# Kernel optimization log

Hardware: AMD Instinct MI355X
Metric: run time of the kernel (lower is better)

The kernel has to match this reference:

```python
import jax, jax.numpy as jnp
import numpy as np

B, T, E = 4, 2048, 2048
H, KV = 16, 4
G = H // KV           # GQA group size
D = E // H            # head_dim = 128


def setup_inputs() -> dict:
    key = jax.random.key(0)
    kx, kq, kk, kv, ko = jax.random.split(key, 5)
    s = 1.0 / np.sqrt(E).astype(np.float32)
    x  = jax.random.normal(kx, (B, T, E), jnp.float32)
    Wq = jax.random.normal(kq, (E, H * D), jnp.float32) * s
    Wk = jax.random.normal(kk, (E, KV * D), jnp.float32) * s
    Wv = jax.random.normal(kv, (E, KV * D), jnp.float32) * s
    Wo = jax.random.normal(ko, (H * D, E), jnp.float32) * s
    return {"x": x, "Wq": Wq, "Wk": Wk, "Wv": Wv, "Wo": Wo}


def reference(x, Wq, Wk, Wv, Wo):
    # causal=True (default in the torch module)
    b, t, _ = x.shape
    scale = 1.0 / np.sqrt(D).astype(np.float32)
    # q heads ordered so that reshape (H,)->(KV,G) matches torch repeat_interleave
    q = (x @ Wq).reshape(b, t, KV, G, D)   # (B,T,KV,G,D)
    k = (x @ Wk).reshape(b, t, KV, D)      # (B,T,KV,D)
    v = (x @ Wv).reshape(b, t, KV, D)
    # scores per (kv-head h, group member g): (B,KV,G,T,T)
    scores = jnp.einsum('bqhgd,bkhd->bhgqk', q, k) * scale
    causal_mask = jnp.tril(jnp.ones((t, t), dtype=bool))  # True = keep
    scores = jnp.where(causal_mask, scores, -jnp.inf)
    w = jax.nn.softmax(scores, axis=-1)
    y = jnp.einsum('bhgqk,bkhd->bqhgd', w, v)  # (B,T,KV,G,D)
    y = y.reshape(b, t, H * D)
    return y @ Wo
```

## Files before the change

### kernel.cpp

```cpp
#include <hip/hip_runtime.h>

typedef unsigned short u16;
typedef __attribute__((ext_vector_type(8))) __bf16 bf16x8;
typedef __attribute__((ext_vector_type(4))) float f32x4;

#define BB 4
#define TT 2048
#define EE 2048
#define HH 16
#define KVH 4
#define DD 128

static __device__ __forceinline__ u16 f2bf(float f) {
  unsigned int u = __float_as_uint(f);
  u += 0x7fffu + ((u >> 16) & 1u);
  return (u16)(u >> 16);
}

static __device__ __forceinline__ void gl_lds16(const u16* g, u16* l) {
  __builtin_amdgcn_global_load_lds((__attribute__((address_space(1))) void*)g,
                                   (__attribute__((address_space(3))) void*)l,
                                   16, 0, 0);
}

__global__ __launch_bounds__(256) void cvt_f32_bf16(const float* __restrict__ in,
                                                    u16* __restrict__ out, int n4) {
  int i = blockIdx.x * 256 + threadIdx.x;
  if (i >= n4) return;
  float4 v = ((const float4*)in)[i];
  union { uint2 u2; u16 s[4]; } o;
  o.s[0] = f2bf(v.x); o.s[1] = f2bf(v.y); o.s[2] = f2bf(v.z); o.s[3] = f2bf(v.w);
  ((uint2*)out)[i] = o.u2;
}

__global__ __launch_bounds__(256) void transpose_w(const float* __restrict__ W,
                                                   u16* __restrict__ Wt, int R, int C) {
  __shared__ float tile[32][33];
  int tx = threadIdx.x & 31, ty = threadIdx.x >> 5;
  int r0 = blockIdx.y * 32, c0 = blockIdx.x * 32;
  #pragma unroll
  for (int i = ty; i < 32; i += 8)
    tile[i][tx] = W[(size_t)(r0 + i) * C + (c0 + tx)];
  __syncthreads();
  #pragma unroll
  for (int i = ty; i < 32; i += 8)
    Wt[(size_t)(c0 + i) * R + (r0 + tx)] = f2bf(tile[tx][i]);
}

__global__ __launch_bounds__(256) void transpose_v(const u16* __restrict__ KVb,
                                                   u16* __restrict__ VTg) {
  __shared__ u16 tile[32][36];
  const int tid = threadIdx.x;
  const int t0 = blockIdx.x * 32, d0 = blockIdx.y * 32;
  const int z = blockIdx.z;
  const int vb = z * 128;
  const size_t srcbase = (size_t)(z >> 2) * TT * 1024 + 512 + (z & 3) * 128;
  {
    int i = tid >> 3, c4 = (tid & 7) * 4;
    union { uint2 u; u16 s[4]; } r;
    r.u = *(const uint2*)(KVb + srcbase + (size_t)(t0 + i) * 1024 + d0 + c4);
    tile[i][c4] = r.s[0]; tile[i][c4 + 1] = r.s[1];
    tile[i][c4 + 2] = r.s[2]; tile[i][c4 + 3] = r.s[3];
  }
  __syncthreads();
  {
    int j = tid >> 3, cc = (tid & 7) * 4;
    union { uint2 u; u16 s[4]; } w;
    w.s[0] = tile[cc][j]; w.s[1] = tile[cc + 1][j];
    w.s[2] = tile[cc + 2][j]; w.s[3] = tile[cc + 3][j];
    *(uint2*)(VTg + (size_t)(vb + d0 + j) * TT + t0 + cc) = w.u;
  }
}

template <int MODE>
__global__ __launch_bounds__(512) void gemm256(const u16* __restrict__ A,
                                               const u16* __restrict__ Bt0,
                                               const u16* __restrict__ Bt1,
                                               void* __restrict__ C0,
                                               void* __restrict__ C1,
                                               int M, int N0, int N1, int K, int nbx) {
  __shared__ __align__(16) u16 sh[2][4][8192];
  const int tid = threadIdx.x;
  const int lane = tid & 63, wave = tid >> 6;
  const int quad = lane >> 4, n16 = lane & 15;
  const int mi = wave >> 2, ni = wave & 3;

  const int nwg = gridDim.x;
  int wg = blockIdx.x;
  wg = (wg & 7) * (nwg >> 3) + (wg >> 3);
  const int bx = wg % nbx, by = wg / nbx;
  const size_t rowbase = (size_t)by * 256;
  const int colbase = bx * 256;

  const u16* Bt = Bt0;
  int bcol = colbase;
  if (MODE == 1 && colbase >= N0) { Bt = Bt1; bcol = colbase - N0; }

  const int c0 = tid, c1 = tid + 512;
  const int r0s = c0 >> 3, ci0 = (c0 & 7) ^ (r0s & 7);
  const int r1s = c1 >> 3, ci1 = (c1 & 7) ^ (r1s & 7);
  const u16* Ag0 = A + (rowbase + r0s) * (size_t)K + ci0 * 8;
  const u16* Ag1 = A + (rowbase + r1s) * (size_t)K + ci1 * 8;
  const u16* Bg0 = Bt + ((size_t)bcol + r0s) * K + ci0 * 8;
  const u16* Bg1 = Bt + ((size_t)bcol + r1s) * K + ci1 * 8;
  const size_t h128K = (size_t)128 * K;

#define STAGE(ob, h, kb) do {                                              \
    if ((h) < 2) {                                                         \
      gl_lds16(Ag0 + (size_t)(h) * h128K + (kb), &sh[ob][h][c0 * 8]);      \
      gl_lds16(Ag1 + (size_t)(h) * h128K + (kb), &sh[ob][h][c1 * 8]);      \
    } else {                                                               \
      gl_lds16(Bg0 + (size_t)((h) - 2) * h128K + (kb), &sh[ob][h][c0 * 8]);\
      gl_lds16(Bg1 + (size_t)((h) - 2) * h128K + (kb), &sh[ob][h][c1 * 8]);\
    } } while (0)

#define LDA_HALF(mh) do {                                                  \
    _Pragma("unroll") for (int m = 0; m < 4; ++m)                          \
      _Pragma("unroll") for (int kk = 0; kk < 2; ++kk) {                   \
        int row_ = ((mh) * 4 + m) * 16 + n16;                              \
        int c_ = row_ * 8 + ((kk * 4 + quad) ^ (n16 & 7));                 \
        af[m][kk] = *(const bf16x8*)&sh[buf][mi][c_ * 8];                  \
      } } while (0)

#define LDB_HALF(nh, BF) do {                                              \
    _Pragma("unroll") for (int n = 0; n < 2; ++n)                          \
      _Pragma("unroll") for (int kk = 0; kk < 2; ++kk) {                   \
        int row_ = (ni & 1) * 64 + ((nh) * 2 + n) * 16 + n16;              \
        int c_ = row_ * 8 + ((kk * 4 + quad) ^ (n16 & 7));                 \
        BF[n][kk] = *(const bf16x8*)&sh[buf][2 + (ni >> 1)][c_ * 8];       \
      } } while (0)

#define DO_QUAD(mh, nh, BF) do {                                           \
    __builtin_amdgcn_s_setprio(1);                                         \
    _Pragma("unroll") for (int m = 0; m < 4; ++m)                          \
      _Pragma("unroll") for (int n = 0; n < 2; ++n)                        \
        _Pragma("unroll") for (int kk = 0; kk < 2; ++kk)                   \
          acc[(mh) * 4 + m][(nh) * 2 + n] =                                \
              __builtin_amdgcn_mfma_f32_16x16x32_bf16(                     \
                  af[m][kk], BF[n][kk], acc[(mh) * 4 + m][(nh) * 2 + n],   \
                  0, 0, 0);                                                \
    __builtin_amdgcn_s_setprio(0);                                         \
  } while (0)

#define FENCE() asm volatile("" ::: "memory")

  f32x4 acc[8][4];
  #pragma unroll
  for (int i = 0; i < 8; ++i)
    #pragma unroll
    for (int j = 0; j < 4; ++j) acc[i][j] = (f32x4){0.f, 0.f, 0.f, 0.f};

  bf16x8 af[4][2], bf0[2][2], bf1[2][2];
  const int nt = K / 64;

  STAGE(0, 0, 0); STAGE(0, 1, 0); STAGE(0, 2, 0); STAGE(0, 3, 0);

  #pragma unroll 2
  for (int t = 0; t < nt; ++t) {
    const int buf = t & 1, ob = buf ^ 1;
    const int kbn = (t + 1) * 64;
    const bool pre = (t + 1 < nt);

    if (pre) {
      STAGE(ob, 0, kbn);
      asm volatile("s_waitcnt vmcnt(2)" ::: "memory");
    } else {
      asm volatile("s_waitcnt vmcnt(0)" ::: "memory");
    }
    __builtin_amdgcn_s_barrier(); FENCE();
    LDA_HALF(0); LDB_HALF(0, bf0);
    DO_QUAD(0, 0, bf0);
    __builtin_amdgcn_s_barrier(); FENCE();

    LDB_HALF(1, bf1);
    if (pre) STAGE(ob, 1, kbn);
    __builtin_amdgcn_s_barrier(); FENCE();
    DO_QUAD(0, 1, bf1);
    __builtin_amdgcn_s_barrier(); FENCE();

    LDA_HALF(1);
    if (pre) STAGE(ob, 2, kbn);
    __builtin_amdgcn_s_barrier(); FENCE();
    DO_QUAD(1, 1, bf1);
    __builtin_amdgcn_s_barrier(); FENCE();

    if (pre) STAGE(ob, 3, kbn);
    __builtin_amdgcn_s_barrier(); FENCE();
    DO_QUAD(1, 0, bf0);
    __builtin_amdgcn_s_barrier(); FENCE();
  }

#undef STAGE
#undef LDA_HALF
#undef LDB_HALF
#undef DO_QUAD
#undef FENCE

  const size_t crow0 = rowbase + (size_t)mi * 128;
  #pragma unroll
  for (int mt = 0; mt < 8; ++mt) {
    #pragma unroll
    for (int r = 0; r < 4; ++r) {
      size_t row = crow0 + mt * 16 + quad * 4 + r;
      #pragma unroll
      for (int nt_ = 0; nt_ < 4; ++nt_) {
        int col = colbase + ni * 64 + nt_ * 16 + n16;
        float v = acc[mt][nt_][r];
        if (MODE == 0) {
          ((float*)C0)[row * (size_t)N0 + col] = v;
        } else {
          if (col < N0) ((u16*)C0)[row * (size_t)N0 + col] = f2bf(v);
          else          ((u16*)C1)[row * (size_t)N1 + (col - N0)] = f2bf(v);
        }
      }
    }
  }
}

template <int MODE>
__global__ __launch_bounds__(512) void gemm_n128(const u16* __restrict__ A,
                                                 const u16* __restrict__ Bt0,
                                                 const u16* __restrict__ Bt1,
                                                 void* __restrict__ C0,
                                                 void* __restrict__ C1,
                                                 int M, int N0, int N1, int K, int nbx) {
  __shared__ __align__(16) u16 sh[2][3][8192];
  const int tid = threadIdx.x;
  const int lane = tid & 63, wave = tid >> 6;
  const int quad = lane >> 4, n16 = lane & 15;
  const int mi = wave >> 1, ni = wave & 1;

  const int nwg = gridDim.x;
  int wg = blockIdx.x;
  wg = (wg & 7) * (nwg >> 3) + (wg >> 3);
  const int bx = wg % nbx, by = wg / nbx;
  const size_t rowbase = (size_t)by * 256;
  const int colbase = bx * 128;

  const u16* Bt = Bt0;
  int bcol = colbase;
  if (MODE == 1 && colbase >= N0) { Bt = Bt1; bcol = colbase - N0; }

  const int c0 = tid, c1 = tid + 512;
  const int r0s = c0 >> 3, ci0 = (c0 & 7) ^ (r0s & 7);
  const int r1s = c1 >> 3, ci1 = (c1 & 7) ^ (r1s & 7);
  const u16* Ag0 = A + (rowbase + r0s) * (size_t)K + ci0 * 8;
  const u16* Ag1 = A + (rowbase + r1s) * (size_t)K + ci1 * 8;
  const u16* Bg0 = Bt + ((size_t)bcol + r0s) * K + ci0 * 8;
  const u16* Bg1 = Bt + ((size_t)bcol + r1s) * K + ci1 * 8;
  const size_t h128K = (size_t)128 * K;

#define STAGEN(ob, h, kb) do {                                             \
    if ((h) < 2) {                                                         \
      gl_lds16(Ag0 + (size_t)(h) * h128K + (kb), &sh[ob][h][c0 * 8]);      \
      gl_lds16(Ag1 + (size_t)(h) * h128K + (kb), &sh[ob][h][c1 * 8]);      \
    } else {                                                               \
      gl_lds16(Bg0 + (kb), &sh[ob][2][c0 * 8]);                            \
      gl_lds16(Bg1 + (kb), &sh[ob][2][c1 * 8]);                            \
    } } while (0)

#define LDAN(mh) do {                                                      \
    _Pragma("unroll") for (int m = 0; m < 2; ++m)                          \
      _Pragma("unroll") for (int kk = 0; kk < 2; ++kk) {                   \
        int row_ = (mi & 1) * 64 + ((mh) * 2 + m) * 16 + n16;              \
        int c_ = row_ * 8 + ((kk * 4 + quad) ^ (n16 & 7));                 \
        af[m][kk] = *(const bf16x8*)&sh[buf][mi >> 1][c_ * 8];             \
      } } while (0)

#define LDBN(nh, BF) do {                                                  \
    _Pragma("unroll") for (int n = 0; n < 2; ++n)                          \
      _Pragma("unroll") for (int kk = 0; kk < 2; ++kk) {                   \
        int row_ = ni * 64 + ((nh) * 2 + n) * 16 + n16;                    \
        int c_ = row_ * 8 + ((kk * 4 + quad) ^ (n16 & 7));                 \
        BF[n][kk] = *(const bf16x8*)&sh[buf][2][c_ * 8];                   \
      } } while (0)

#define QUADN(mh, nh, BF) do {                                             \
    __builtin_amdgcn_s_setprio(1);                                         \
    _Pragma("unroll") for (int m = 0; m < 2; ++m)                          \
      _Pragma("unroll") for (int n = 0; n < 2; ++n)                        \
        _Pragma("unroll") for (int kk = 0; kk < 2; ++kk)                   \
          acc[(mh) * 2 + m][(nh) * 2 + n] =                                \
              __builtin_amdgcn_mfma_f32_16x16x32_bf16(                     \
                  af[m][kk], BF[n][kk], acc[(mh) * 2 + m][(nh) * 2 + n],   \
                  0, 0, 0);                                                \
    __builtin_amdgcn_s_setprio(0);                                         \
  } while (0)

#define FENCE() asm volatile("" ::: "memory")

  f32x4 acc[4][4];
  #pragma unroll
  for (int i = 0; i < 4; ++i)
    #pragma unroll
    for (int j = 0; j < 4; ++j) acc[i][j] = (f32x4){0.f, 0.f, 0.f, 0.f};

  bf16x8 af[2][2], bf0[2][2], bf1[2][2];
  const int nt = K / 64;

  STAGEN(0, 0, 0); STAGEN(0, 1, 0); STAGEN(0, 2, 0);

  #pragma unroll 2
  for (int t = 0; t < nt; ++t) {
    const int buf = t & 1, ob = buf ^ 1;
    const int kbn = (t + 1) * 64;
    const bool pre = (t + 1 < nt);

    if (pre) {
      STAGEN(ob, 0, kbn);
      asm volatile("s_waitcnt vmcnt(2)" ::: "memory");
    } else {
      asm volatile("s_waitcnt vmcnt(0)" ::: "memory");
    }
    __builtin_amdgcn_s_barrier(); FENCE();
    LDAN(0); LDBN(0, bf0);
    QUADN(0, 0, bf0);
    __builtin_amdgcn_s_barrier(); FENCE();

    LDBN(1, bf1);
    if (pre) STAGEN(ob, 1, kbn);
    __builtin_amdgcn_s_barrier(); FENCE();
    QUADN(0, 1, bf1);
    __builtin_amdgcn_s_barrier(); FENCE();

    LDAN(1);
    if (pre) STAGEN(ob, 2, kbn);
    __builtin_amdgcn_s_barrier(); FENCE();
    QUADN(1, 1, bf1);
    __builtin_amdgcn_s_barrier(); FENCE();

    __builtin_amdgcn_s_barrier(); FENCE();
    QUADN(1, 0, bf0);
    __builtin_amdgcn_s_barrier(); FENCE();
  }

#undef STAGEN
#undef LDAN
#undef LDBN
#undef QUADN
#undef FENCE

  const size_t crow0 = rowbase + (size_t)mi * 64;
  #pragma unroll
  for (int mt = 0; mt < 4; ++mt) {
    #pragma unroll
    for (int r = 0; r < 4; ++r) {
      size_t row = crow0 + mt * 16 + quad * 4 + r;
      #pragma unroll
      for (int nt_ = 0; nt_ < 4; ++nt_) {
        int col = colbase + ni * 64 + nt_ * 16 + n16;
        float v = acc[mt][nt_][r];
        if (MODE == 0) {
          ((float*)C0)[row * (size_t)N0 + col] = v;
        } else {
          if (col < N0) ((u16*)C0)[row * (size_t)N0 + col] = f2bf(v);
          else          ((u16*)C1)[row * (size_t)N1 + (col - N0)] = f2bf(v);
        }
      }
    }
  }
}

__global__ __launch_bounds__(256) void attn_kernel(const u16* __restrict__ Qm,
                                                   const u16* __restrict__ KVm,
                                                   const u16* __restrict__ VTg,
                                                   u16* __restrict__ Ym) {
  __shared__ u16 Ks[32 * 128];
  __shared__ u16 Vt[128 * 32];
  __shared__ u16 Pb[4 * 32 * 40];

  const int tid = threadIdx.x;
  const int lane = tid & 63, wave = tid >> 6;
  const int quad = lane >> 4, n16 = lane & 15;
  const int b = blockIdx.y >> 4, h = blockIdx.y & 15;
  const int kvh = h >> 2;
  const int kvbase = b * TT;
  const u16* VTg_ = VTg + (size_t)((b * 4 + kvh) * 128) * TT;

  const int krow = tid >> 4, kslot = tid & 15;
  const int kg = (kslot ^ krow) * 8;
  u16* Ksd0 = &Ks[krow * 128 + kslot * 8];
  u16* Ksd1 = &Ks[(krow + 16) * 128 + kslot * 8];
  const int vrow = tid >> 2, vs = tid & 3;
  const int vq8 = (vs ^ ((tid >> 3) & 3)) * 8;
  u16* Vtd0 = &Vt[vrow * 32 + vs * 8];
  u16* Vtd1 = &Vt[(vrow + 64) * 32 + vs * 8];

  constexpr float SCL = 0.08838834764831843f * 1.4426950408889634f;

  for (int pass = 0; pass < 2; ++pass) {
    const int qt = pass ? 15 - (int)blockIdx.x : (int)blockIdx.x;
    const int q0 = qt * 128;
    const size_t qrowbase = (size_t)(b * TT + q0);
    const int wq0 = wave * 32;

    bf16x8 aq[2][4];
    #pragma unroll
    for (int mt = 0; mt < 2; ++mt) {
      const u16* qp = Qm + (qrowbase + wq0 + mt * 16 + n16) * (HH * DD) + h * DD + quad * 8;
      #pragma unroll
      for (int dt = 0; dt < 4; ++dt)
        aq[mt][dt] = *(const bf16x8*)(qp + dt * 32);
    }

    float lrow[2][4];
    f32x4 oacc[2][8];
    #pragma unroll
    for (int mt = 0; mt < 2; ++mt) {
      #pragma unroll
      for (int r = 0; r < 4; ++r) lrow[mt][r] = 0.f;
      #pragma unroll
      for (int i = 0; i < 8; ++i) oacc[mt][i] = (f32x4){0.f, 0.f, 0.f, 0.f};
    }

    const int kend = q0 + 128;
    for (int kb = 0; kb < kend; kb += 32) {
      __syncthreads();
      gl_lds16(KVm + (size_t)(kvbase + kb + krow) * 1024 + kvh * DD + kg, Ksd0);
      gl_lds16(KVm + (size_t)(kvbase + kb + krow + 16) * 1024 + kvh * DD + kg, Ksd1);
      gl_lds16(VTg_ + (size_t)vrow * TT + kb + vq8, Vtd0);
      gl_lds16(VTg_ + (size_t)(vrow + 64) * TT + kb + vq8, Vtd1);
      __syncthreads();

      f32x4 sf[2][2];
      #pragma unroll
      for (int half = 0; half < 2; ++half) {
        bf16x8 bk[4];
        #pragma unroll
        for (int dt = 0; dt < 4; ++dt) {
          int slot = (dt * 4 + quad) ^ n16;
          bk[dt] = *(const bf16x8*)&Ks[(half * 16 + n16) * 128 + slot * 8];
        }
        #pragma unroll
        for (int mt = 0; mt < 2; ++mt) {
          f32x4 s = (f32x4){0.f, 0.f, 0.f, 0.f};
          #pragma unroll
          for (int dt = 0; dt < 4; ++dt)
            s = __builtin_amdgcn_mfma_f32_16x16x32_bf16(aq[mt][dt], bk[dt], s, 0, 0, 0);
          sf[mt][half] = s;
        }
      }

      u16* pw = &Pb[wave * (32 * 40)];
      #pragma unroll
      for (int mt = 0; mt < 2; ++mt)
        #pragma unroll
        for (int half = 0; half < 2; ++half) {
          int key = kb + half * 16 + n16;
          #pragma unroll
          for (int r = 0; r < 4; ++r) {
            int qpos = q0 + wq0 + mt * 16 + quad * 4 + r;
            float pv = (key <= qpos) ? exp2f(sf[mt][half][r] * SCL) : 0.f;
            lrow[mt][r] += pv;
            pw[(mt * 16 + quad * 4 + r) * 40 + half * 16 + n16] = f2bf(pv);
          }
        }
      __builtin_amdgcn_s_waitcnt(0);
      bf16x8 ap[2];
      ap[0] = *(const bf16x8*)&pw[n16 * 40 + quad * 8];
      ap[1] = *(const bf16x8*)&pw[(16 + n16) * 40 + quad * 8];

      #pragma unroll
      for (int dt = 0; dt < 8; ++dt) {
        bf16x8 bv = *(const bf16x8*)&Vt[(dt * 16 + n16) * 32 +
                                        ((quad ^ ((n16 >> 1) & 3)) * 8)];
        oacc[0][dt] = __builtin_amdgcn_mfma_f32_16x16x32_bf16(ap[0], bv, oacc[0][dt], 0, 0, 0);
        oacc[1][dt] = __builtin_amdgcn_mfma_f32_16x16x32_bf16(ap[1], bv, oacc[1][dt], 0, 0, 0);
      }
    }

    float rinv[2][4];
    #pragma unroll
    for (int mt = 0; mt < 2; ++mt)
      #pragma unroll
      for (int r = 0; r < 4; ++r) {
        float v = lrow[mt][r];
        v += __shfl_xor(v, 1, 64);
        v += __shfl_xor(v, 2, 64);
        v += __shfl_xor(v, 4, 64);
        v += __shfl_xor(v, 8, 64);
        rinv[mt][r] = 1.0f / v;
      }
    #pragma unroll
    for (int mt = 0; mt < 2; ++mt)
      #pragma unroll
      for (int dt = 0; dt < 8; ++dt)
        #pragma unroll
        for (int r = 0; r < 4; ++r) {
          size_t row = qrowbase + wq0 + mt * 16 + quad * 4 + r;
          Ym[row * (HH * DD) + h * DD + dt * 16 + n16] = f2bf(oacc[mt][dt][r] * rinv[mt][r]);
        }
  }
}

extern "C" void kernel_launch(void* const* d_in, const int* in_sizes, int n_in,
                              void* d_out, int out_size, void* d_ws, size_t ws_size,
                              hipStream_t stream) {
  const float* x  = (const float*)d_in[0];
  const float* Wq = (const float*)d_in[1];
  const float* Wk = (const float*)d_in[2];
  const float* Wv = (const float*)d_in[3];
  const float* Wo = (const float*)d_in[4];
  float* out = (float*)d_out;

  u16* ws   = (u16*)d_ws;
  u16* xb   = ws;
  u16* Wbuf = xb + (size_t)8192 * 2048;
  u16* Yb   = xb;

  u16* ob   = (u16*)d_out;
  u16* Qb   = ob;
  u16* KVb  = ob + (size_t)8192 * 2048;
  u16* VTg  = ob + (size_t)8192 * 2048 + (size_t)8192 * 1024;
  u16* WkvT = VTg + (size_t)16 * 128 * 2048;

  cvt_f32_bf16<<<16384, 256, 0, stream>>>(x, xb, (4 * 2048 * 2048) / 4);

  transpose_w<<<dim3(64, 64), 256, 0, stream>>>(Wq, Wbuf, 2048, 2048);
  transpose_w<<<dim3(16, 64), 256, 0, stream>>>(Wk, WkvT, 2048, 512);
  transpose_w<<<dim3(16, 64), 256, 0, stream>>>(Wv, WkvT + (size_t)512 * 2048, 2048, 512);

  gemm_n128<1><<<768, 512, 0, stream>>>(xb, Wbuf, WkvT, (void*)Qb, (void*)KVb,
                                        8192, 2048, 1024, 2048, 24);

  transpose_v<<<dim3(64, 4, 16), 256, 0, stream>>>(KVb, VTg);

  attn_kernel<<<dim3(8, 64), 256, 0, stream>>>(Qb, KVb, VTg, Yb);

  transpose_w<<<dim3(64, 64), 256, 0, stream>>>(Wo, Wbuf, 2048, 2048);
  gemm256<0><<<256, 512, 0, stream>>>(Yb, Wbuf, nullptr, (void*)out, nullptr,
                                      8192, 2048, 0, 2048, 8);
}
```

Baseline: 470.7 us.

## Replace 256x256 output-projection GEMM with 256x128 K32 double-buffered kernel

The output projection GEMM (8192x2048x2048) now uses a new kernel with 256x128 tiles and K-step 32 instead of the 256x256, K-step 64 kernel. LDS use drops to 48 KB and launch bounds request 4 blocks per CU. The grid doubles to 512 workgroups, which gives better CU fill on the chip and more occupancy to hide latency. In exchange, each output element gets less data reuse and a barrier is paid every 32-wide K step.

```diff
diff --git a/kernel.cpp b/kernel.cpp
--- a/kernel.cpp
+++ b/kernel.cpp
@@ -73,151 +73,6 @@
 }
 
 template <int MODE>
-__global__ __launch_bounds__(512) void gemm256(const u16* __restrict__ A,
-                                               const u16* __restrict__ Bt0,
-                                               const u16* __restrict__ Bt1,
-                                               void* __restrict__ C0,
-                                               void* __restrict__ C1,
-                                               int M, int N0, int N1, int K, int nbx) {
-  __shared__ __align__(16) u16 sh[2][4][8192];
-  const int tid = threadIdx.x;
-  const int lane = tid & 63, wave = tid >> 6;
-  const int quad = lane >> 4, n16 = lane & 15;
-  const int mi = wave >> 2, ni = wave & 3;
-
-  const int nwg = gridDim.x;
-  int wg = blockIdx.x;
-  wg = (wg & 7) * (nwg >> 3) + (wg >> 3);
-  const int bx = wg % nbx, by = wg / nbx;
-  const size_t rowbase = (size_t)by * 256;
-  const int colbase = bx * 256;
-
-  const u16* Bt = Bt0;
-  int bcol = colbase;
-  if (MODE == 1 && colbase >= N0) { Bt = Bt1; bcol = colbase - N0; }
-
-  const int c0 = tid, c1 = tid + 512;
-  const int r0s = c0 >> 3, ci0 = (c0 & 7) ^ (r0s & 7);
-  const int r1s = c1 >> 3, ci1 = (c1 & 7) ^ (r1s & 7);
-  const u16* Ag0 = A + (rowbase + r0s) * (size_t)K + ci0 * 8;
-  const u16* Ag1 = A + (rowbase + r1s) * (size_t)K + ci1 * 8;
-  const u16* Bg0 = Bt + ((size_t)bcol + r0s) * K + ci0 * 8;
-  const u16* Bg1 = Bt + ((size_t)bcol + r1s) * K + ci1 * 8;
-  const size_t h128K = (size_t)128 * K;
-
-#define STAGE(ob, h, kb) do {                                              \
-    if ((h) < 2) {                                                         \
-      gl_lds16(Ag0 + (size_t)(h) * h128K + (kb), &sh[ob][h][c0 * 8]);      \
-      gl_lds16(Ag1 + (size_t)(h) * h128K + (kb), &sh[ob][h][c1 * 8]);      \
-    } else {                                                               \
-      gl_lds16(Bg0 + (size_t)((h) - 2) * h128K + (kb), &sh[ob][h][c0 * 8]);\
-      gl_lds16(Bg1 + (size_t)((h) - 2) * h128K + (kb), &sh[ob][h][c1 * 8]);\
-    } } while (0)
-
-#define LDA_HALF(mh) do {                                                  \
-    _Pragma("unroll") for (int m = 0; m < 4; ++m)                          \
-      _Pragma("unroll") for (int kk = 0; kk < 2; ++kk) {                   \
-        int row_ = ((mh) * 4 + m) * 16 + n16;                              \
-        int c_ = row_ * 8 + ((kk * 4 + quad) ^ (n16 & 7));                 \
-        af[m][kk] = *(const bf16x8*)&sh[buf][mi][c_ * 8];                  \
-      } } while (0)
-
-#define LDB_HALF(nh, BF) do {                                              \
-    _Pragma("unroll") for (int n = 0; n < 2; ++n)                          \
-      _Pragma("unroll") for (int kk = 0; kk < 2; ++kk) {                   \
-        int row_ = (ni & 1) * 64 + ((nh) * 2 + n) * 16 + n16;              \
-        int c_ = row_ * 8 + ((kk * 4 + quad) ^ (n16 & 7));                 \
-        BF[n][kk] = *(const bf16x8*)&sh[buf][2 + (ni >> 1)][c_ * 8];       \
-      } } while (0)
-
-#define DO_QUAD(mh, nh, BF) do {                                           \
-    __builtin_amdgcn_s_setprio(1);                                         \
-    _Pragma("unroll") for (int m = 0; m < 4; ++m)                          \
-      _Pragma("unroll") for (int n = 0; n < 2; ++n)                        \
-        _Pragma("unroll") for (int kk = 0; kk < 2; ++kk)                   \
-          acc[(mh) * 4 + m][(nh) * 2 + n] =                                \
-              __builtin_amdgcn_mfma_f32_16x16x32_bf16(                     \
-                  af[m][kk], BF[n][kk], acc[(mh) * 4 + m][(nh) * 2 + n],   \
-                  0, 0, 0);                                                \
-    __builtin_amdgcn_s_setprio(0);                                         \
-  } while (0)
-
-#define FENCE() asm volatile("" ::: "memory")
-
-  f32x4 acc[8][4];
-  #pragma unroll
-  for (int i = 0; i < 8; ++i)
-    #pragma unroll
-    for (int j = 0; j < 4; ++j) acc[i][j] = (f32x4){0.f, 0.f, 0.f, 0.f};
-
-  bf16x8 af[4][2], bf0[2][2], bf1[2][2];
-  const int nt = K / 64;
-
-  STAGE(0, 0, 0); STAGE(0, 1, 0); STAGE(0, 2, 0); STAGE(0, 3, 0);
-
-  #pragma unroll 2
-  for (int t = 0; t < nt; ++t) {
-    const int buf = t & 1, ob = buf ^ 1;
-    const int kbn = (t + 1) * 64;
-    const bool pre = (t + 1 < nt);
-
-    if (pre) {
-      STAGE(ob, 0, kbn);
-      asm volatile("s_waitcnt vmcnt(2)" ::: "memory");
-    } else {
-      asm volatile("s_waitcnt vmcnt(0)" ::: "memory");
-    }
-    __builtin_amdgcn_s_barrier(); FENCE();
-    LDA_HALF(0); LDB_HALF(0, bf0);
-    DO_QUAD(0, 0, bf0);
-    __builtin_amdgcn_s_barrier(); FENCE();
-
-    LDB_HALF(1, bf1);
-    if (pre) STAGE(ob, 1, kbn);
-    __builtin_amdgcn_s_barrier(); FENCE();
-    DO_QUAD(0, 1, bf1);
-    __builtin_amdgcn_s_barrier(); FENCE();
-
-    LDA_HALF(1);
-    if (pre) STAGE(ob, 2, kbn);
-    __builtin_amdgcn_s_barrier(); FENCE();
-    DO_QUAD(1, 1, bf1);
-    __builtin_amdgcn_s_barrier(); FENCE();
-
-    if (pre) STAGE(ob, 3, kbn);
-    __builtin_amdgcn_s_barrier(); FENCE();
-    DO_QUAD(1, 0, bf0);
-    __builtin_amdgcn_s_barrier(); FENCE();
-  }
-
-#undef STAGE
-#undef LDA_HALF
-#undef LDB_HALF
-#undef DO_QUAD
-#undef FENCE
-
-  const size_t crow0 = rowbase + (size_t)mi * 128;
-  #pragma unroll
-  for (int mt = 0; mt < 8; ++mt) {
-    #pragma unroll
-    for (int r = 0; r < 4; ++r) {
-      size_t row = crow0 + mt * 16 + quad * 4 + r;
-      #pragma unroll
-      for (int nt_ = 0; nt_ < 4; ++nt_) {
-        int col = colbase + ni * 64 + nt_ * 16 + n16;
-        float v = acc[mt][nt_][r];
-        if (MODE == 0) {
-          ((float*)C0)[row * (size_t)N0 + col] = v;
-        } else {
-          if (col < N0) ((u16*)C0)[row * (size_t)N0 + col] = f2bf(v);
-          else          ((u16*)C1)[row * (size_t)N1 + (col - N0)] = f2bf(v);
-        }
-      }
-    }
-  }
-}
-
-template <int MODE>
 __global__ __launch_bounds__(512) void gemm_n128(const u16* __restrict__ A,
                                                  const u16* __restrict__ Bt0,
                                                  const u16* __restrict__ Bt1,
@@ -356,6 +211,99 @@
           if (col < N0) ((u16*)C0)[row * (size_t)N0 + col] = f2bf(v);
           else          ((u16*)C1)[row * (size_t)N1 + (col - N0)] = f2bf(v);
         }
+      }
+    }
+  }
+}
+
+__global__ __launch_bounds__(512, 4) void gemm_k32(const u16* __restrict__ A,
+                                                   const u16* __restrict__ Bt,
+                                                   float* __restrict__ C,
+                                                   int M, int N, int K, int nbx) {
+  __shared__ __align__(16) u16 sh[2][3][4096];
+  const int tid = threadIdx.x;
+  const int lane = tid & 63, wave = tid >> 6;
+  const int quad = lane >> 4, n16 = lane & 15;
+  const int mi = wave >> 1, ni = wave & 1;
+
+  const int nwg = gridDim.x;
+  int wg = blockIdx.x;
+  wg = (wg & 7) * (nwg >> 3) + (wg >> 3);
+  const int bx = wg % nbx, by = wg / nbx;
+  const size_t rowbase = (size_t)by * 256;
+  const int colbase = bx * 128;
+
+  const int srow = tid >> 2, sci = (tid & 3) ^ ((tid >> 3) & 3);
+  const u16* Ag0 = A + (rowbase + srow) * (size_t)K + sci * 8;
+  const u16* Ag1 = A + (rowbase + 128 + srow) * (size_t)K + sci * 8;
+  const u16* Bg  = Bt + ((size_t)colbase + srow) * K + sci * 8;
+
+#define STAGEK(ob, kb) do {                                                \
+    gl_lds16(Ag0 + (kb), &sh[ob][0][tid * 8]);                             \
+    gl_lds16(Ag1 + (kb), &sh[ob][1][tid * 8]);                             \
+    gl_lds16(Bg  + (kb), &sh[ob][2][tid * 8]);                             \
+  } while (0)
+
+#define FENCE() asm volatile("" ::: "memory")
+
+  f32x4 acc[4][4];
+  #pragma unroll
+  for (int i = 0; i < 4; ++i)
+    #pragma unroll
+    for (int j = 0; j < 4; ++j) acc[i][j] = (f32x4){0.f, 0.f, 0.f, 0.f};
+
+  const int nt = K / 32;
+  STAGEK(0, 0);
+
+  #pragma unroll 2
+  for (int t = 0; t < nt; ++t) {
+    const int buf = t & 1, ob = buf ^ 1;
+    if (t + 1 < nt) {
+      STAGEK(ob, (t + 1) * 32);
+      asm volatile("s_waitcnt vmcnt(3)" ::: "memory");
+    } else {
+      asm volatile("s_waitcnt vmcnt(0)" ::: "memory");
+    }
+    __builtin_amdgcn_s_barrier(); FENCE();
+
+    bf16x8 af[4], bf[4];
+    #pragma unroll
+    for (int m = 0; m < 4; ++m) {
+      int row_ = (mi & 1) * 64 + m * 16 + n16;
+      int c_ = row_ * 4 + (quad ^ ((row_ >> 1) & 3));
+      af[m] = *(const bf16x8*)&sh[buf][mi >> 1][c_ * 8];
+    }
+    #pragma unroll
+    for (int n = 0; n < 4; ++n) {
+      int row_ = ni * 64 + n * 16 + n16;
+      int c_ = row_ * 4 + (quad ^ ((row_ >> 1) & 3));
+      bf[n] = *(const bf16x8*)&sh[buf][2][c_ * 8];
+    }
+
+    __builtin_amdgcn_s_setprio(1);
+    #pragma unroll
+    for (int m = 0; m < 4; ++m)
+      #pragma unroll
+      for (int n = 0; n < 4; ++n)
+        acc[m][n] = __builtin_amdgcn_mfma_f32_16x16x32_bf16(af[m], bf[n], acc[m][n], 0, 0, 0);
+    __builtin_amdgcn_s_setprio(0);
+
+    FENCE(); __builtin_amdgcn_s_barrier(); FENCE();
+  }
+
+#undef STAGEK
+#undef FENCE
+
+  const size_t crow0 = rowbase + (size_t)mi * 64;
+  #pragma unroll
+  for (int mt = 0; mt < 4; ++mt) {
+    #pragma unroll
+    for (int r = 0; r < 4; ++r) {
+      size_t row = crow0 + mt * 16 + quad * 4 + r;
+      #pragma unroll
+      for (int nt_ = 0; nt_ < 4; ++nt_) {
+        int col = colbase + ni * 64 + nt_ * 16 + n16;
+        C[row * (size_t)N + col] = acc[mt][nt_][r];
       }
     }
   }
@@ -528,6 +476,5 @@
   attn_kernel<<<dim3(8, 64), 256, 0, stream>>>(Qb, KVb, VTg, Yb);
 
   transpose_w<<<dim3(64, 64), 256, 0, stream>>>(Wo, Wbuf, 2048, 2048);
-  gemm256<0><<<256, 512, 0, stream>>>(Yb, Wbuf, nullptr, (void*)out, nullptr,
-                                      8192, 2048, 0, 2048, 8);
-}
+  gemm_k32<<<512, 512, 0, stream>>>(Yb, Wbuf, out, 8192, 2048, 2048, 16);
+}
```

After: 469.8 us. No clear change (-0.2%).
